# Kernel tuning notes

Hardware: AMD Instinct MI355X
Metric: run time of the kernel (lower is better)

The kernel has to match this reference:

```python
import jax, jax.numpy as jnp
import numpy as np

N_HEAD = 32


def _apply_rope(x, rope):
    # x: (B, H, T, hs); rope: (block_size, hs//2) angles
    B, H, T, hs = x.shape
    ang = rope[:T]  # (T, hs//2)
    cos = jnp.cos(ang)[None, :, None, :]  # (1, T, 1, hs//2)
    sin = jnp.sin(ang)[None, :, None, :]
    xt = x.transpose(0, 2, 1, 3).reshape(B, T, H, hs // 2, 2)
    x0, x1 = xt[..., 0], xt[..., 1]
    out_r = x0 * cos - x1 * sin
    out_i = x0 * sin + x1 * cos
    out = jnp.stack([out_r, out_i], axis=-1).reshape(B, T, H, hs)
    return out.transpose(0, 2, 1, 3)


def setup_inputs() -> dict:
    key = jax.random.key(0)
    ks = jax.random.split(key, 6)
    B, T, C = 2, 2048, 4096
    aT = 10
    hs = C // N_HEAD
    return {
        "x": jax.random.normal(ks[0], (B, T, C), dtype=jnp.float32),
        "adaption_prompt": jax.random.normal(ks[1], (1, aT, C), dtype=jnp.float32),
        "rope_cache": jax.random.uniform(ks[2], (4096, hs // 2), dtype=jnp.float32) * 2.0 * np.pi,
        "w_attn": jax.random.normal(ks[3], (C, 3 * C), dtype=jnp.float32) * 0.02,
        "w_proj": jax.random.normal(ks[4], (C, C), dtype=jnp.float32) * 0.02,
        "gating_factor": jax.random.normal(ks[5], (1,), dtype=jnp.float32) * 0.1,
    }


def reference(x, adaption_prompt, rope_cache, w_attn, w_proj, gating_factor):
    B, T, C = x.shape
    H = N_HEAD
    hs = C // H

    qkv = x @ w_attn  # (B, T, 3C)
    q, k, v = jnp.split(qkv, 3, axis=2)
    q = q.reshape(B, T, H, hs).transpose(0, 2, 1, 3)  # (B, H, T, hs)
    k = k.reshape(B, T, H, hs).transpose(0, 2, 1, 3)
    v = v.reshape(B, T, H, hs).transpose(0, 2, 1, 3)

    q = _apply_rope(q, rope_cache)
    k = _apply_rope(k, rope_cache)

    # causal SDPA, scale = 1/sqrt(head_size)
    scale = 1.0 / jnp.sqrt(jnp.asarray(hs, dtype=q.dtype))
    scores = jnp.einsum("bhqd,bhkd->bhqk", q, k) * scale
    causal = jnp.tril(jnp.ones((T, T), dtype=bool))
    scores = jnp.where(causal[None, None, :, :], scores, jnp.asarray(-jnp.inf, scores.dtype))
    attn = jax.nn.softmax(scores, axis=-1)
    y = jnp.einsum("bhqk,bhkd->bhqd", attn, v)  # (B, H, T, hs)

    # adapter attention (note: scale uses full n_embd, as in source)
    aT = adaption_prompt.shape[1]
    aqkv = adaption_prompt @ w_attn  # (1, aT, 3C)
    _, ak, av = jnp.split(aqkv, 3, axis=2)
    ak = ak.reshape(1, aT, H, hs).transpose(0, 2, 1, 3)  # (1, H, aT, hs)
    av = av.reshape(1, aT, H, hs).transpose(0, 2, 1, 3)
    ascores = jnp.einsum("bhqd,xhkd->bhqk", q, ak) / jnp.sqrt(jnp.asarray(C, q.dtype))
    ascores = gating_factor[0] * jax.nn.softmax(ascores.astype(jnp.float32), axis=-1).astype(q.dtype)
    y = y + jnp.einsum("bhqk,xhkd->bhqd", ascores, av)

    y = y.transpose(0, 2, 1, 3).reshape(B, T, C)
    return y @ w_proj
```

## Files before the change

kernel.cpp:

```cpp
#include <hip/hip_runtime.h>

typedef unsigned short u16;
typedef unsigned int u32;
typedef __attribute__((ext_vector_type(4))) float f32x4;
typedef __attribute__((ext_vector_type(8))) _Float16 half8;
typedef __attribute__((ext_vector_type(8))) unsigned short u16x8;
typedef __attribute__((ext_vector_type(4))) unsigned short u16x4;

static __device__ __forceinline__ u16 f2h(float f) {
  union { _Float16 h; u16 u; } c;
  c.h = (_Float16)f;
  return c.u;
}
static __device__ __forceinline__ float h2f(u16 u) {
  union { _Float16 h; u16 u; } c;
  c.u = u;
  return (float)c.h;
}
static __device__ __forceinline__ void gload_lds16(const void* g, void* l) {
  __builtin_amdgcn_global_load_lds((const __attribute__((address_space(1))) void*)g,
                                   (__attribute__((address_space(3))) void*)l,
                                   16, 0, 0);
}

__global__ __launch_bounds__(256) void transpose_cvt(const float* __restrict__ src,
                                                     u16* __restrict__ dst,
                                                     int R, int C) {
  __shared__ float tile[32][33];
  const int tx = threadIdx.x, ty = threadIdx.y;
  const int c0 = blockIdx.x << 5, r0 = blockIdx.y << 5;
#pragma unroll
  for (int i = 0; i < 32; i += 8)
    tile[ty + i][tx] = src[(size_t)(r0 + ty + i) * C + c0 + tx];
  __syncthreads();
#pragma unroll
  for (int i = 0; i < 32; i += 8)
    dst[(size_t)(c0 + ty + i) * R + r0 + tx] = f2h(tile[tx][ty + i]);
}

__global__ __launch_bounds__(256) void cvt_f32_f16(const float* __restrict__ in,
                                                   u16* __restrict__ out, int n4) {
  int i = blockIdx.x * 256 + threadIdx.x;
  if (i >= n4) return;
  f32x4 v = *(const f32x4*)(in + (size_t)i * 4);
  u16x4 o;
  o[0] = f2h(v[0]); o[1] = f2h(v[1]); o[2] = f2h(v[2]); o[3] = f2h(v[3]);
  *(u16x4*)(out + (size_t)i * 4) = o;
}

static __device__ __forceinline__ void store_out(float* C, size_t idx, float v) { C[idx] = v; }
static __device__ __forceinline__ void store_out(u16* C, size_t idx, float v) { C[idx] = f2h(v); }

static __device__ __forceinline__ void stageA(const u16* __restrict__ Ab, int K, int kt,
                                              u16* As, int mh, int t) {
  int hf = t >> 8;
  int tt = t & 255;
  int row = hf * 128 + mh * 32 + (tt >> 3);
  int slot = tt & 7;
  gload_lds16(Ab + (size_t)row * K + kt + ((slot ^ (row & 7)) << 3),
              (char*)As + hf * 16384 + mh * 4096 + tt * 16);
}
static __device__ __forceinline__ void stageB(const u16* __restrict__ Bb, int K, int kt,
                                              u16* Bs, int j, int t) {
  int row = j * 64 + (t >> 3);
  int slot = t & 7;
  gload_lds16(Bb + (size_t)row * K + kt + ((slot ^ (row & 7)) << 3),
              (char*)Bs + j * 8192 + t * 16);
}

#define LOAD_BF(BS)                                                              \
  _Pragma("unroll") for (int nf = 0; nf < 4; ++nf)                               \
    _Pragma("unroll") for (int kk = 0; kk < 2; ++kk) {                           \
      int row = wn * 64 + nf * 16 + l15;                                         \
      int slot = (kk * 4 + g) ^ (l15 & 7);                                       \
      bf[nf][kk] = *(const half8*)((const char*)(BS) + row * 128 + slot * 16);   \
    }

#define DO_PHASE(AS, Q, STAGE_STMT, WAIT_STR)                                    \
  {                                                                              \
    half8 af[2][2];                                                              \
    _Pragma("unroll") for (int mf = 0; mf < 2; ++mf)                             \
      _Pragma("unroll") for (int kk = 0; kk < 2; ++kk) {                         \
        int row = wm * 128 + ((Q) * 2 + mf) * 16 + l15;                          \
        int slot = (kk * 4 + g) ^ (l15 & 7);                                     \
        af[mf][kk] = *(const half8*)((const char*)(AS) + row * 128 + slot * 16); \
      }                                                                          \
    STAGE_STMT;                                                                  \
    asm volatile("s_barrier" ::: "memory");                                      \
    __builtin_amdgcn_s_setprio(1);                                               \
    _Pragma("unroll") for (int kk = 0; kk < 2; ++kk)                             \
      _Pragma("unroll") for (int mf = 0; mf < 2; ++mf)                           \
        _Pragma("unroll") for (int nf = 0; nf < 4; ++nf)                         \
          acc[(Q) * 2 + mf][nf] = __builtin_amdgcn_mfma_f32_16x16x32_f16(        \
              af[mf][kk], bf[nf][kk], acc[(Q) * 2 + mf][nf], 0, 0, 0);           \
    __builtin_amdgcn_s_setprio(0);                                               \
    asm volatile(WAIT_STR ::: "memory");                                         \
  }

template <typename OutT>
__global__ __launch_bounds__(512, 2) void gemm256(const u16* __restrict__ A,
                                                  const u16* __restrict__ Bt,
                                                  OutT* __restrict__ C,
                                                  int M, int N, int K, int nbn) {
  __shared__ u16 lds[4][16384];
  const int t = threadIdx.x;
  const int lane = t & 63;
  const int wid = t >> 6;
  const int g = lane >> 4, l15 = lane & 15;
  const int wm = wid >> 2, wn = wid & 3;
  const int nwg = gridDim.x;
  const int bid = blockIdx.x;
  const int wgid = (bid & 7) * (nwg >> 3) + (bid >> 3);
  const int bm = wgid / nbn, bn = wgid % nbn;
  const u16* Ab = A + (size_t)bm * 256 * K;
  const u16* Bb = Bt + (size_t)bn * 256 * K;
  f32x4 acc[8][4] = {};

  stageA(Ab, K, 0, lds[0], 0, t);
  stageB(Bb, K, 0, lds[1], 0, t);
  stageB(Bb, K, 0, lds[1], 1, t);
  stageB(Bb, K, 0, lds[1], 2, t);
  stageB(Bb, K, 0, lds[1], 3, t);
  stageA(Ab, K, 0, lds[0], 1, t);
  stageA(Ab, K, 0, lds[0], 2, t);
  stageA(Ab, K, 0, lds[0], 3, t);
  stageB(Bb, K, 64, lds[3], 0, t);
  stageB(Bb, K, 64, lds[3], 1, t);
  stageA(Ab, K, 64, lds[2], 0, t);
  stageA(Ab, K, 64, lds[2], 1, t);
  asm volatile("s_waitcnt vmcnt(7)\ns_barrier" ::: "memory");

  const int nt = K >> 6;
  for (int i = 0; i < nt; ++i) {
    u16* As = lds[(i & 1) << 1];
    u16* Bs = lds[((i & 1) << 1) + 1];
    u16* Asn = lds[((i + 1) & 1) << 1];
    u16* Bsn = lds[(((i + 1) & 1) << 1) + 1];
    int k1 = (i + 1) << 6; if (k1 >= K) k1 = 0;
    int k2 = (i + 2) << 6; if (k2 >= K) k2 = 0;
    half8 bf[4][2];
    LOAD_BF(Bs);
    DO_PHASE(As, 0, { stageB(Bb, K, k1, Bsn, 2, t); stageB(Bb, K, k1, Bsn, 3, t); },
             "s_waitcnt vmcnt(8)\ns_barrier");
    DO_PHASE(As, 1, { stageA(Ab, K, k1, Asn, 2, t); stageA(Ab, K, k1, Asn, 3, t); },
             "s_waitcnt vmcnt(8)\ns_barrier");
    DO_PHASE(As, 2, { stageB(Bb, K, k2, Bs, 0, t); stageB(Bb, K, k2, Bs, 1, t); },
             "s_barrier");
    DO_PHASE(As, 3, { stageA(Ab, K, k2, As, 0, t); stageA(Ab, K, k2, As, 1, t); },
             "s_waitcnt vmcnt(6)\ns_barrier");
  }
  asm volatile("s_waitcnt vmcnt(0)" ::: "memory");

#pragma unroll
  for (int mf = 0; mf < 8; ++mf) {
    int row0 = bm * 256 + wm * 128 + mf * 16 + 4 * g;
#pragma unroll
    for (int nf = 0; nf < 4; ++nf) {
      int col = bn * 256 + wn * 64 + nf * 16 + l15;
#pragma unroll
      for (int r = 0; r < 4; ++r)
        store_out(C, (size_t)(row0 + r) * N + col, acc[mf][nf][r]);
    }
  }
}

__global__ __launch_bounds__(256) void rope_kernel(u16* __restrict__ qkv,
                                                   const float* __restrict__ rope) {
  int idx = blockIdx.x * 256 + threadIdx.x;
  int bt = idx >> 12;
  int pp = idx & 4095;
  int part = pp >> 11;
  int within = pp & 2047;
  int hh = within >> 6;
  int p = within & 63;
  int tpos = bt & 2047;
  size_t off = (size_t)bt * 12288 + part * 4096 + hh * 128 + 2 * p;
  u32* ptr = (u32*)(qkv + off);
  u32 v = *ptr;
  float x0 = h2f((u16)(v & 0xffff));
  float x1 = h2f((u16)(v >> 16));
  float sn, cs;
  __sincosf(rope[tpos * 64 + p], &sn, &cs);
  float y0 = x0 * cs - x1 * sn;
  float y1 = x0 * sn + x1 * cs;
  *ptr = (u32)f2h(y0) | ((u32)f2h(y1) << 16);
}

__global__ __launch_bounds__(256) void v_transpose(const u16* __restrict__ qkv,
                                                   u16* __restrict__ vt) {
  __shared__ u16 tile[64 * 128];
  const int bx = blockIdx.x;
  const int tt = bx & 31, h = (bx >> 5) & 31, b = bx >> 10;
  const u16* src = qkv + (size_t)b * 2048 * 12288 + 8192 + h * 128;
  const int t = threadIdx.x;
#pragma unroll
  for (int i = 0; i < 4; ++i) {
    int c = t + 256 * i;
    int row = c >> 4, slot = c & 15;
    u16x8 v = *(const u16x8*)(src + (size_t)(tt * 64 + row) * 12288 + slot * 8);
    *(u16x8*)(tile + row * 128 + ((slot ^ (row >> 3)) << 3)) = v;
  }
  __syncthreads();
  u16* dst = vt + (size_t)(b * 32 + h) * 128 * 2048 + tt * 64;
#pragma unroll
  for (int i = 0; i < 4; ++i) {
    int c = t + 256 * i;
    int drow = c >> 3, t8 = c & 7;
    u16x8 o;
#pragma unroll
    for (int e = 0; e < 8; ++e) {
      int row = t8 * 8 + e;
      int slot = (drow >> 3) ^ (row >> 3);
      o[e] = tile[row * 128 + (slot << 3) + (drow & 7)];
    }
    *(u16x8*)(dst + (size_t)drow * 2048 + t8 * 8) = o;
  }
}

__global__ __launch_bounds__(256) void adaption_kv_kernel(const float* __restrict__ prompt,
                                                          const float* __restrict__ w_attn,
                                                          u16* __restrict__ akbuf,
                                                          u16* __restrict__ avbuf) {
  __shared__ float pl[10][512];
  __shared__ float red[8][10][32];
  const int t = threadIdx.x;
  const int tc = t & 31, tk = t >> 5;
  const int n = blockIdx.x * 32 + tc;
  float acc[10] = {};
  for (int k0 = 0; k0 < 4096; k0 += 512) {
    __syncthreads();
#pragma unroll
    for (int i = 0; i < 20; ++i) {
      int idx = t + 256 * i;
      int j = idx >> 9, kk = idx & 511;
      pl[j][kk] = prompt[(size_t)j * 4096 + k0 + kk];
    }
    __syncthreads();
    for (int kk = tk; kk < 512; kk += 8) {
      float wv = w_attn[(size_t)(k0 + kk) * 12288 + 4096 + n];
#pragma unroll
      for (int j = 0; j < 10; ++j) acc[j] += pl[j][kk] * wv;
    }
  }
  __syncthreads();
#pragma unroll
  for (int j = 0; j < 10; ++j) red[tk][j][tc] = acc[j];
  __syncthreads();
  if (tk == 0) {
    float s[10];
#pragma unroll
    for (int j = 0; j < 10; ++j) {
      s[j] = 0.f;
#pragma unroll
      for (int q = 0; q < 8; ++q) s[j] += red[q][j][tc];
    }
    u16* dst;
    int hh, d;
    if (n < 4096) { dst = akbuf; hh = n >> 7; d = n & 127; }
    else          { dst = avbuf; hh = (n - 4096) >> 7; d = n & 127; }
#pragma unroll
    for (int j = 0; j < 16; ++j)
      dst[(size_t)(hh * 16 + j) * 128 + d] = (j < 10) ? f2h(s[j]) : (u16)0;
  }
}

__global__ __launch_bounds__(256) void attn_kernel(const u16* __restrict__ qkv,
                                                   const u16* __restrict__ vt,
                                                   const u16* __restrict__ akbuf,
                                                   const u16* __restrict__ avbuf,
                                                   const float* __restrict__ gating,
                                                   u16* __restrict__ y) {
  __shared__ u16 Kl[64 * 128];
  __shared__ u16 Vtl[128 * 64];
  __shared__ u16 Pl[4][16 * 64];

  const int t = threadIdx.x;
  const int lane = t & 63, w = t >> 6;
  const int g = lane >> 4, l15 = lane & 15;
  const int bx = blockIdx.x;
  const int qb = 31 - (bx >> 6);
  const int bh = bx & 63, b = bh >> 5, h = bh & 31;
  const int ldq = 12288;
  const u16* Qg = qkv + (size_t)b * 2048 * ldq + h * 128;
  const u16* Kg = Qg + 4096;
  const u16* VtG = vt + (size_t)(b * 32 + h) * 128 * 2048;
  u16* AKb = &Pl[0][0];

#pragma unroll
  for (int i = 0; i < 4; ++i) {
    int c = t + 256 * i;
    int row = c >> 4, slot = c & 15;
    gload_lds16(Qg + (size_t)(qb * 64 + row) * ldq + ((slot ^ (row & 15)) << 3),
                (char*)Kl + c * 16);
  }
  {
    int row = t >> 4, slot = t & 15;
    gload_lds16(akbuf + (size_t)(h * 16 + row) * 128 + ((slot ^ row) << 3),
                (char*)AKb + t * 16);
  }
  __syncthreads();

  half8 qf[4];
#pragma unroll
  for (int kk = 0; kk < 4; ++kk) {
    int slot = (kk * 4 + g) ^ l15;
    qf[kk] = *(const half8*)((const char*)Kl + (w * 16 + l15) * 256 + (slot << 4));
  }
  f32x4 sa = {};
#pragma unroll
  for (int kk = 0; kk < 4; ++kk) {
    int slot = (kk * 4 + g) ^ l15;
    half8 af = *(const half8*)((const char*)AKb + l15 * 256 + (slot << 4));
    sa = __builtin_amdgcn_mfma_f32_16x16x32_f16(qf[kk], af, sa, 0, 0, 0);
  }
  __syncthreads();

  f32x4 acc[8] = {};
  float mrun[4], lrun[4];
#pragma unroll
  for (int r = 0; r < 4; ++r) { mrun[r] = -1e30f; lrun[r] = 0.f; }

  for (int kvt = 0; kvt <= qb; ++kvt) {
#pragma unroll
    for (int i = 0; i < 4; ++i) {
      int c = t + 256 * i;
      int row = c >> 4, slot = c & 15;
      gload_lds16(Kg + (size_t)(kvt * 64 + row) * ldq + ((slot ^ (row & 15)) << 3),
                  (char*)Kl + c * 16);
    }
#pragma unroll
    for (int i = 0; i < 4; ++i) {
      int c = t + 256 * i;
      int d = c >> 3, s3 = c & 7;
      gload_lds16(VtG + (size_t)d * 2048 + kvt * 64 + ((s3 ^ (d & 7)) << 3),
                  (char*)Vtl + c * 16);
    }
    __syncthreads();

    f32x4 s[4] = {};
#pragma unroll
    for (int nf = 0; nf < 4; ++nf) {
#pragma unroll
      for (int kk = 0; kk < 4; ++kk) {
        int slot = (kk * 4 + g) ^ l15;
        half8 kf = *(const half8*)((const char*)Kl + (nf * 16 + l15) * 256 + (slot << 4));
        s[nf] = __builtin_amdgcn_mfma_f32_16x16x32_f16(qf[kk], kf, s[nf], 0, 0, 0);
      }
    }
    const float sc = 0.08838834764831843f;
    if (kvt == qb) {
#pragma unroll
      for (int nf = 0; nf < 4; ++nf)
#pragma unroll
        for (int r = 0; r < 4; ++r) {
          int kv = nf * 16 + l15;
          int qq = w * 16 + 4 * g + r;
          float v = s[nf][r] * sc;
          s[nf][r] = (kv <= qq) ? v : -1e30f;
        }
    } else {
#pragma unroll
      for (int nf = 0; nf < 4; ++nf)
#pragma unroll
        for (int r = 0; r < 4; ++r) s[nf][r] *= sc;
    }

    float alpha[4];
#pragma unroll
    for (int r = 0; r < 4; ++r) {
      float mt = fmaxf(fmaxf(s[0][r], s[1][r]), fmaxf(s[2][r], s[3][r]));
#pragma unroll
      for (int off = 1; off < 16; off <<= 1)
        mt = fmaxf(mt, __shfl_xor(mt, off, 64));
      float mn = fmaxf(mrun[r], mt);
      alpha[r] = __expf(mrun[r] - mn);
      mrun[r] = mn;
      float rs = 0.f;
#pragma unroll
      for (int nf = 0; nf < 4; ++nf) {
        float p = __expf(s[nf][r] - mn);
        s[nf][r] = p;
        rs += p;
      }
#pragma unroll
      for (int off = 1; off < 16; off <<= 1)
        rs += __shfl_xor(rs, off, 64);
      lrun[r] = lrun[r] * alpha[r] + rs;
    }
#pragma unroll
    for (int nd = 0; nd < 8; ++nd)
#pragma unroll
      for (int r = 0; r < 4; ++r)
        acc[nd][r] *= alpha[r];

#pragma unroll
    for (int nf = 0; nf < 4; ++nf)
#pragma unroll
      for (int r = 0; r < 4; ++r) {
        int qq = 4 * g + r;
        int kv = nf * 16 + l15;
        int byteoff = (qq * 128 + kv * 2) ^ ((qq & 7) << 4);
        *(u16*)((char*)Pl[w] + byteoff) = f2h(s[nf][r]);
      }

#pragma unroll
    for (int kk2 = 0; kk2 < 2; ++kk2) {
      int pslot = (kk2 * 4 + g) ^ (l15 & 7);
      half8 pf = *(const half8*)((const char*)Pl[w] + l15 * 128 + (pslot << 4));
#pragma unroll
      for (int nd = 0; nd < 8; ++nd) {
        int d = nd * 16 + l15;
        int slot = (kk2 * 4 + g) ^ (d & 7);
        half8 vf = *(const half8*)((const char*)Vtl + d * 128 + (slot << 4));
        acc[nd] = __builtin_amdgcn_mfma_f32_16x16x32_f16(pf, vf, acc[nd], 0, 0, 0);
      }
    }
    __syncthreads();
  }

  {
    int d = t >> 1;
    int jb = (t & 1) << 4;
#pragma unroll
    for (int i = 0; i < 16; ++i) {
      int j = jb + i;
      u16 v = (j < 16) ? avbuf[(size_t)(h * 16 + j) * 128 + d] : (u16)0;
      int byteoff = (d * 64 + j * 2) ^ ((d & 3) << 4);
      *(u16*)((char*)Kl + byteoff) = v;
    }
  }
  __syncthreads();

  float ga = gating[0];
  float pa4[4];
#pragma unroll
  for (int r = 0; r < 4; ++r) {
    float v = sa[r] * (1.0f / 64.0f);
    if (l15 >= 10) v = -1e30f;
    float mt = v;
#pragma unroll
    for (int off = 1; off < 16; off <<= 1)
      mt = fmaxf(mt, __shfl_xor(mt, off, 64));
    float p = __expf(v - mt);
    float rs = p;
#pragma unroll
    for (int off = 1; off < 16; off <<= 1)
      rs += __shfl_xor(rs, off, 64);
    pa4[r] = p / rs * ga;
  }
#pragma unroll
  for (int r = 0; r < 4; ++r) {
    float inv = 1.0f / lrun[r];
#pragma unroll
    for (int nd = 0; nd < 8; ++nd)
      acc[nd][r] *= inv;
  }
#pragma unroll
  for (int r = 0; r < 4; ++r) {
    int qq = 4 * g + r;
    int b1 = (qq * 128 + l15 * 2) ^ ((qq & 7) << 4);
    *(u16*)((char*)Pl[w] + b1) = f2h(pa4[r]);
    int b2 = (qq * 128 + (16 + l15) * 2) ^ ((qq & 7) << 4);
    *(u16*)((char*)Pl[w] + b2) = 0;
  }
  {
    int pslot = g ^ (l15 & 7);
    half8 pf = *(const half8*)((const char*)Pl[w] + l15 * 128 + (pslot << 4));
#pragma unroll
    for (int nd = 0; nd < 8; ++nd) {
      int d = nd * 16 + l15;
      int byteoff = (d * 64 + g * 16) ^ ((d & 3) << 4);
      half8 avf = *(const half8*)((const char*)Kl + byteoff);
      acc[nd] = __builtin_amdgcn_mfma_f32_16x16x32_f16(pf, avf, acc[nd], 0, 0, 0);
    }
  }
#pragma unroll
  for (int nd = 0; nd < 8; ++nd) {
    int col = h * 128 + nd * 16 + l15;
#pragma unroll
    for (int r = 0; r < 4; ++r) {
      int row = qb * 64 + w * 16 + 4 * g + r;
      y[(size_t)(b * 2048 + row) * 4096 + col] = f2h(acc[nd][r]);
    }
  }
}

extern "C" void kernel_launch(void* const* d_in, const int* in_sizes, int n_in,
                              void* d_out, int out_size, void* d_ws, size_t ws_size,
                              hipStream_t stream) {
  (void)in_sizes; (void)n_in; (void)out_size; (void)ws_size;
  const float* x      = (const float*)d_in[0];
  const float* prompt = (const float*)d_in[1];
  const float* rope   = (const float*)d_in[2];
  const float* w_attn = (const float*)d_in[3];
  const float* w_proj = (const float*)d_in[4];
  const float* gating = (const float*)d_in[5];
  float* out = (float*)d_out;

  char* ws = (char*)d_ws;
  u16* WtA = (u16*)(ws);
  u16* Yb  = (u16*)(ws);
  u16* VtG = (u16*)(ws + 33554432);
  u16* qkv = (u16*)(ws + 100663296);
  u16* xb  = (u16*)(ws + 201326592);
  u16* WtP = (u16*)(ws + 201326592);
  u16* akb = (u16*)(ws + 234881024);
  u16* avb = (u16*)(ws + 234881024 + 131072);

  transpose_cvt<<<dim3(384, 128), dim3(32, 8), 0, stream>>>(w_attn, WtA, 4096, 12288);
  cvt_f32_f16<<<dim3(16384), dim3(256), 0, stream>>>(x, xb, 4194304);
  gemm256<u16><<<dim3(768), dim3(512), 0, stream>>>(xb, WtA, qkv, 4096, 12288, 4096, 48);
  rope_kernel<<<dim3(65536), dim3(256), 0, stream>>>(qkv, rope);
  v_transpose<<<dim3(2048), dim3(256), 0, stream>>>(qkv, VtG);
  adaption_kv_kernel<<<dim3(256), dim3(256), 0, stream>>>(prompt, w_attn, akb, avb);
  attn_kernel<<<dim3(2048), dim3(256), 0, stream>>>(qkv, VtG, akb, avb, gating, Yb);
  transpose_cvt<<<dim3(128, 128), dim3(32, 8), 0, stream>>>(w_proj, WtP, 4096, 4096);
  gemm256<float><<<dim3(256), dim3(512), 0, stream>>>(Yb, WtP, out, 4096, 4096, 4096, 16);
}
```

Measured before the change: 1.012 ms.

## Restructure GEMM main loop to simple double buffering with one barrier per tile

Replaces the 4-phase ping-pong schedule, which used several barriers per K-tile and partial vmcnt waits, with a simpler double-buffered loop. Each iteration issues all global-to-LDS loads for the next tile at the start, interleaves A-fragment LDS reads with MFMA bursts through register double-buffering, then waits for everything and barriers once. This cuts barrier and synchronisation overhead, but it shortens the prefetch distance from two tiles to one and fully drains vmcnt every iteration, so memory latency may be exposed.

```diff
diff --git a/kernel.cpp b/kernel.cpp
--- a/kernel.cpp
+++ b/kernel.cpp
@@ -76,26 +76,22 @@
       bf[nf][kk] = *(const half8*)((const char*)(BS) + row * 128 + slot * 16);   \
     }
 
-#define DO_PHASE(AS, Q, STAGE_STMT, WAIT_STR)                                    \
-  {                                                                              \
-    half8 af[2][2];                                                              \
+#define LOAD_AF(AF, AS, Q)                                                       \
+  _Pragma("unroll") for (int mf = 0; mf < 2; ++mf)                               \
+    _Pragma("unroll") for (int kk = 0; kk < 2; ++kk) {                           \
+      int row = wm * 128 + ((Q) * 2 + mf) * 16 + l15;                            \
+      int slot = (kk * 4 + g) ^ (l15 & 7);                                       \
+      (AF)[mf][kk] = *(const half8*)((const char*)(AS) + row * 128 + slot * 16); \
+    }
+
+#define MFMA_BURST(AF, Q)                                                        \
+  __builtin_amdgcn_s_setprio(1);                                                 \
+  _Pragma("unroll") for (int kk = 0; kk < 2; ++kk)                               \
     _Pragma("unroll") for (int mf = 0; mf < 2; ++mf)                             \
-      _Pragma("unroll") for (int kk = 0; kk < 2; ++kk) {                         \
-        int row = wm * 128 + ((Q) * 2 + mf) * 16 + l15;                          \
-        int slot = (kk * 4 + g) ^ (l15 & 7);                                     \
-        af[mf][kk] = *(const half8*)((const char*)(AS) + row * 128 + slot * 16); \
-      }                                                                          \
-    STAGE_STMT;                                                                  \
-    asm volatile("s_barrier" ::: "memory");                                      \
-    __builtin_amdgcn_s_setprio(1);                                               \
-    _Pragma("unroll") for (int kk = 0; kk < 2; ++kk)                             \
-      _Pragma("unroll") for (int mf = 0; mf < 2; ++mf)                           \
-        _Pragma("unroll") for (int nf = 0; nf < 4; ++nf)                         \
-          acc[(Q) * 2 + mf][nf] = __builtin_amdgcn_mfma_f32_16x16x32_f16(        \
-              af[mf][kk], bf[nf][kk], acc[(Q) * 2 + mf][nf], 0, 0, 0);           \
-    __builtin_amdgcn_s_setprio(0);                                               \
-    asm volatile(WAIT_STR ::: "memory");                                         \
-  }
+      _Pragma("unroll") for (int nf = 0; nf < 4; ++nf)                           \
+        acc[(Q) * 2 + mf][nf] = __builtin_amdgcn_mfma_f32_16x16x32_f16(          \
+            (AF)[mf][kk], bf[nf][kk], acc[(Q) * 2 + mf][nf], 0, 0, 0);           \
+  __builtin_amdgcn_s_setprio(0);
 
 template <typename OutT>
 __global__ __launch_bounds__(512, 2) void gemm256(const u16* __restrict__ A,
@@ -117,39 +113,44 @@
   f32x4 acc[8][4] = {};
 
   stageA(Ab, K, 0, lds[0], 0, t);
+  stageA(Ab, K, 0, lds[0], 1, t);
+  stageA(Ab, K, 0, lds[0], 2, t);
+  stageA(Ab, K, 0, lds[0], 3, t);
   stageB(Bb, K, 0, lds[1], 0, t);
   stageB(Bb, K, 0, lds[1], 1, t);
   stageB(Bb, K, 0, lds[1], 2, t);
   stageB(Bb, K, 0, lds[1], 3, t);
-  stageA(Ab, K, 0, lds[0], 1, t);
-  stageA(Ab, K, 0, lds[0], 2, t);
-  stageA(Ab, K, 0, lds[0], 3, t);
-  stageB(Bb, K, 64, lds[3], 0, t);
-  stageB(Bb, K, 64, lds[3], 1, t);
-  stageA(Ab, K, 64, lds[2], 0, t);
-  stageA(Ab, K, 64, lds[2], 1, t);
-  asm volatile("s_waitcnt vmcnt(7)\ns_barrier" ::: "memory");
+  asm volatile("s_waitcnt vmcnt(0)" ::: "memory");
+  __builtin_amdgcn_s_barrier();
 
   const int nt = K >> 6;
   for (int i = 0; i < nt; ++i) {
-    u16* As = lds[(i & 1) << 1];
-    u16* Bs = lds[((i & 1) << 1) + 1];
+    u16* As  = lds[(i & 1) << 1];
+    u16* Bs  = lds[((i & 1) << 1) + 1];
     u16* Asn = lds[((i + 1) & 1) << 1];
     u16* Bsn = lds[(((i + 1) & 1) << 1) + 1];
     int k1 = (i + 1) << 6; if (k1 >= K) k1 = 0;
-    int k2 = (i + 2) << 6; if (k2 >= K) k2 = 0;
-    half8 bf[4][2];
+    half8 bf[4][2], afA[2][2], afB[2][2];
     LOAD_BF(Bs);
-    DO_PHASE(As, 0, { stageB(Bb, K, k1, Bsn, 2, t); stageB(Bb, K, k1, Bsn, 3, t); },
-             "s_waitcnt vmcnt(8)\ns_barrier");
-    DO_PHASE(As, 1, { stageA(Ab, K, k1, Asn, 2, t); stageA(Ab, K, k1, Asn, 3, t); },
-             "s_waitcnt vmcnt(8)\ns_barrier");
-    DO_PHASE(As, 2, { stageB(Bb, K, k2, Bs, 0, t); stageB(Bb, K, k2, Bs, 1, t); },
-             "s_barrier");
-    DO_PHASE(As, 3, { stageA(Ab, K, k2, As, 0, t); stageA(Ab, K, k2, As, 1, t); },
-             "s_waitcnt vmcnt(6)\ns_barrier");
-  }
-  asm volatile("s_waitcnt vmcnt(0)" ::: "memory");
+    LOAD_AF(afA, As, 0);
+    stageB(Bb, K, k1, Bsn, 0, t);
+    stageB(Bb, K, k1, Bsn, 1, t);
+    stageB(Bb, K, k1, Bsn, 2, t);
+    stageB(Bb, K, k1, Bsn, 3, t);
+    stageA(Ab, K, k1, Asn, 0, t);
+    stageA(Ab, K, k1, Asn, 1, t);
+    stageA(Ab, K, k1, Asn, 2, t);
+    stageA(Ab, K, k1, Asn, 3, t);
+    LOAD_AF(afB, As, 1);
+    MFMA_BURST(afA, 0);
+    LOAD_AF(afA, As, 2);
+    MFMA_BURST(afB, 1);
+    LOAD_AF(afB, As, 3);
+    MFMA_BURST(afA, 2);
+    MFMA_BURST(afB, 3);
+    asm volatile("s_waitcnt vmcnt(0) lgkmcnt(0)" ::: "memory");
+    __builtin_amdgcn_s_barrier();
+  }
 
 #pragma unroll
   for (int mf = 0; mf < 8; ++mf) {
```

After: 999.4 us. Within noise of the previous version (-1.2%).
